# Kernel tuning notes

Hardware: AMD Instinct MI355X
Metric: run time of the kernel (lower is better)

The kernel has to match this reference:

```python
import jax, jax.numpy as jnp
import numpy as np

H = 4       # num_heads
K = 16      # neighbors
EPS = 1e-5  # BatchNorm eps (eval mode with running stats)


def _bn1d(y, g, b, m, v):
    # y: [B, C, N]; per-channel affine batchnorm (eval mode)
    return (y - m[:, None]) * (g[:, None] / jnp.sqrt(v[:, None] + EPS)) + b[:, None]


def setup_inputs() -> dict:
    key = jax.random.key(0)
    ks = jax.random.split(key, 10)
    B, C, N = 2, 256, 4096
    s = 0.02
    inp = {
        'x': jax.random.normal(ks[0], (B, C, N), jnp.float32),
        'xyz': jax.random.normal(ks[1], (B, 3, N), jnp.float32),
        'Wq': jax.random.normal(ks[2], (C, C), jnp.float32) * s,
        'Wkv': jax.random.normal(ks[3], (2 * C, C), jnp.float32) * s,
        'Wproj': jax.random.normal(ks[4], (C, C), jnp.float32) * s,
        'rp_w1': jax.random.normal(ks[5], (C, 3), jnp.float32) * s,
        'rp_g': jnp.ones((C,), jnp.float32),
        'rp_b': jnp.zeros((C,), jnp.float32),
        'rp_m': jnp.zeros((C,), jnp.float32),
        'rp_v': jnp.ones((C,), jnp.float32),
        'rp_w2': jax.random.normal(ks[6], (C, C), jnp.float32) * s,
        'bn1_g': jnp.ones((C,), jnp.float32), 'bn1_b': jnp.zeros((C,), jnp.float32),
        'bn1_m': jnp.zeros((C,), jnp.float32), 'bn1_v': jnp.ones((C,), jnp.float32),
        'bn2_g': jnp.ones((C,), jnp.float32), 'bn2_b': jnp.zeros((C,), jnp.float32),
        'bn2_m': jnp.zeros((C,), jnp.float32), 'bn2_v': jnp.ones((C,), jnp.float32),
        'ffn_w1': jax.random.normal(ks[7], (4 * C, C), jnp.float32) * s,
        'ffn_b1': jnp.zeros((4 * C,), jnp.float32),
        'ffn_w2': jax.random.normal(ks[8], (C, 4 * C), jnp.float32) * s,
        'ffn_b2': jnp.zeros((C,), jnp.float32),
    }
    return inp


def reference(x, xyz, Wq, Wkv, Wproj, rp_w1, rp_g, rp_b, rp_m, rp_v, rp_w2,
              bn1_g, bn1_b, bn1_m, bn1_v, bn2_g, bn2_b, bn2_m, bn2_v,
              ffn_w1, ffn_b1, ffn_w2, ffn_b2):
    B, C, N = x.shape
    d = C // H
    scale = d ** -0.5

    # --- KNN indices ---
    pts = xyz.transpose(0, 2, 1)                       # [B,N,3]
    sq = jnp.sum(pts * pts, -1)                        # [B,N]
    dists = sq[:, :, None] + sq[:, None, :] - 2.0 * jnp.einsum('bnc,bmc->bnm', pts, pts)
    idx = jax.lax.top_k(-dists, K)[1]                  # [B,N,K]

    # --- q, k, v (1x1 conv == matmul over channels) ---
    q = jnp.einsum('oc,bcn->bon', Wq, x).reshape(B, H, d, N)
    kv = jnp.einsum('oc,bcn->bon', Wkv, x)
    kf = kv[:, :C].transpose(0, 2, 1)                  # [B,N,C]
    vf = kv[:, C:].transpose(0, 2, 1)                  # [B,N,C]

    gather = jax.vmap(lambda f, i: f[i])               # per-batch KNN gather
    kg = gather(kf, idx).reshape(B, N, K, H, d)
    vg = gather(vf, idx).reshape(B, N, K, H, d)

    # --- attention logits: per-neighbor dot ---
    logits = jnp.einsum('bhdn,bnkhd->bhnk', q, kg) * scale

    # --- relative-position bias (1x1 conv MLP over rel coords) ---
    nbr = gather(pts, idx)                             # [B,N,K,3]
    rel = nbr - pts[:, :, None, :]                     # [B,N,K,3]
    h1 = jnp.einsum('oc,bnkc->bnko', rp_w1, rel)
    h1 = (h1 - rp_m) * (rp_g / jnp.sqrt(rp_v + EPS)) + rp_b
    h1 = jax.nn.relu(h1)
    h2 = jnp.einsum('oc,bnkc->bnko', rp_w2, h1).reshape(B, N, K, H, d)
    logits = logits + jnp.einsum('bnkhd->bhnk', h2)    # sum over d

    attn = jax.nn.softmax(logits, axis=-1)             # [B,H,N,K]
    out = jnp.einsum('bhnk,bnkhd->bhdn', attn, vg).reshape(B, C, N)
    out = jnp.einsum('oc,bcn->bon', Wproj, out)

    x1 = _bn1d(x + out, bn1_g, bn1_b, bn1_m, bn1_v)
    h = jax.nn.relu(jnp.einsum('oc,bcn->bon', ffn_w1, x1) + ffn_b1[:, None])
    f = jnp.einsum('oc,bcn->bon', ffn_w2, h) + ffn_b2[:, None]
    return _bn1d(x1 + f, bn2_g, bn2_b, bn2_m, bn2_v)
```

## Files before the change

### kernel.cpp

```cpp
#include <hip/hip_runtime.h>
#include <math.h>

#define BB   2
#define CC   256
#define NPT  4096
#define HH   4
#define DD   64
#define KNN  16
#define EPSBN 1e-5f

typedef __attribute__((ext_vector_type(8))) short short8;
typedef __attribute__((ext_vector_type(4))) float f32x4;

typedef __attribute__((address_space(3))) unsigned int lds_u32;
typedef const __attribute__((address_space(1))) unsigned int glb_u32;
__device__ __forceinline__ void gl_lds16(const void* g, void* l) {
  __builtin_amdgcn_global_load_lds((glb_u32*)g, (lds_u32*)l, 16, 0, 0);
}

__device__ __forceinline__ unsigned short f2b(float f) {
  union { float f; unsigned int u; } v; v.f = f;
  unsigned int r = (v.u + 0x7FFFu + ((v.u >> 16) & 1u)) >> 16;
  return (unsigned short)r;
}
__device__ __forceinline__ void up2(unsigned int u, float& a, float& b) {
  union { unsigned int x; float f; } lo, hi;
  lo.x = u << 16; hi.x = u & 0xffff0000u;
  a = lo.f; b = hi.f;
}
__device__ __forceinline__ void up16(uint4 u0, uint4 u1, float* f) {
  up2(u0.x, f[0], f[1]);  up2(u0.y, f[2], f[3]);
  up2(u0.z, f[4], f[5]);  up2(u0.w, f[6], f[7]);
  up2(u1.x, f[8], f[9]);  up2(u1.y, f[10], f[11]);
  up2(u1.z, f[12], f[13]); up2(u1.w, f[14], f[15]);
}

__device__ __forceinline__ unsigned int med3u(unsigned int a, unsigned int b, unsigned int c) {
  unsigned int d;
  asm("v_med3_u32 %0, %1, %2, %3" : "=v"(d) : "v"(a), "v"(b), "v"(c));
  return d;
}

__device__ __forceinline__
void wcast_body(const float* Wq, const float* Wkv, const float* Wp,
                const float* W1, const float* W2,
                unsigned short* oQKV, unsigned short* oP,
                unsigned short* o1, unsigned short* o2,
                const float* rp_w1, const float* rp_g, const float* rp_b,
                const float* rp_m, const float* rp_v, const float* rp_w2,
                float4* w1f, float4* W2t, int blk) {
  if (blk == 3072) {
    int c = threadIdx.x;
    float s  = rp_g[c] / sqrtf(rp_v[c] + EPSBN);
    float b0 = rp_b[c] - rp_m[c] * s;
    w1f[c] = make_float4(rp_w1[c*3+0]*s, rp_w1[c*3+1]*s, rp_w1[c*3+2]*s, b0);
    float a0=0.f,a1=0.f,a2=0.f,a3=0.f;
    for (int o = 0; o < 64; o++) {
      a0 += rp_w2[(      o)*CC + c];
      a1 += rp_w2[( 64 + o)*CC + c];
      a2 += rp_w2[(128 + o)*CC + c];
      a3 += rp_w2[(192 + o)*CC + c];
    }
    W2t[c] = make_float4(a0,a1,a2,a3);
    return;
  }
  int i = blk * 256 + threadIdx.x;
  if (i < 65536)        oQKV[i] = f2b(Wq[i]);
  else if (i < 196608)  oQKV[i] = f2b(Wkv[i - 65536]);
  else if (i < 262144)  oP[i - 196608] = f2b(Wp[i - 196608]);
  else if (i < 524288)  o1[i - 262144] = f2b(W1[i - 262144]);
  else                  o2[i - 524288] = f2b(W2[i - 524288]);
}

__device__ __forceinline__
void xcast_body(const float* x, unsigned short* xb, float* xf,
                float (*T)[65], int bx, int by, int bz) {
  int n0 = bx * 64, c0 = by * 64, bb = bz;
  int tid = threadIdx.x;
  {
    int crow = tid >> 2, ns = (tid & 3) * 16;
    const float* xp = x + ((size_t)(bb*CC + c0 + crow))*NPT + n0 + ns;
#pragma unroll
    for (int i = 0; i < 4; i++) {
      float4 v = ((const float4*)xp)[i];
      T[crow][ns + i*4 + 0] = v.x; T[crow][ns + i*4 + 1] = v.y;
      T[crow][ns + i*4 + 2] = v.z; T[crow][ns + i*4 + 3] = v.w;
    }
  }
  __syncthreads();
  {
    int nrow = tid >> 2, cs = (tid & 3) * 16;
    float vals[16];
#pragma unroll
    for (int i = 0; i < 16; i++) vals[i] = T[cs + i][nrow];
    size_t orow = ((size_t)(bb*NPT + n0 + nrow))*CC + c0 + cs;
#pragma unroll
    for (int i = 0; i < 4; i++)
      *(float4*)&xf[orow + i*4] = make_float4(vals[i*4], vals[i*4+1], vals[i*4+2], vals[i*4+3]);
    unsigned short us[16];
#pragma unroll
    for (int i = 0; i < 16; i++) us[i] = f2b(vals[i]);
    *(uint4*)&xb[orow]     = *(const uint4*)&us[0];
    *(uint4*)&xb[orow + 8] = *(const uint4*)&us[8];
  }
}

#define MPROC(M4, MI) { \
    float nd = fmaf(qx2, (M4).x, fmaf(qy2, (M4).y, fmaf(qz2, (M4).z, (M4).w + qsq))); \
    nd = fmaxf(nd, 0.f); \
    unsigned int key = (__float_as_uint(nd) & 0xFFFFFE00u) | (unsigned int)(MI); \
    k15 = med3u(key, k14, k15); k14 = med3u(key, k13, k14); \
    k13 = med3u(key, k12, k13); k12 = med3u(key, k11, k12); \
    k11 = med3u(key, k10, k11); k10 = med3u(key, k9,  k10); \
    k9  = med3u(key, k8,  k9 ); k8  = med3u(key, k7,  k8 ); \
    k7  = med3u(key, k6,  k7 ); k6  = med3u(key, k5,  k6 ); \
    k5  = med3u(key, k4,  k5 ); k4  = med3u(key, k3,  k4 ); \
    k3  = med3u(key, k2,  k3 ); k2  = med3u(key, k1,  k2 ); \
    k1  = med3u(key, k0,  k1 ); k0  = min(key, k0); }

__device__ __forceinline__
void knn_partial_body(const float* xyz, unsigned int* Pp, float4* sp,
                      int s, int qg, int b) {
  const float* base = xyz + (size_t)b * 3 * NPT;
  int c0 = s * 512;
  for (int i = threadIdx.x; i < 512; i += 256) {
    float mx = base[c0 + i], my = base[NPT + c0 + i], mz = base[2*NPT + c0 + i];
    sp[i] = make_float4(mx, my, mz, mx*mx + my*my + mz*mz);
  }
  int lane = threadIdx.x & 63;
  int wv   = threadIdx.x >> 6;
  int qn   = qg * 64 + lane;
  float qx = base[qn], qy = base[NPT + qn], qz = base[2*NPT + qn];
  float qsq = qx*qx + qy*qy + qz*qz;
  float qx2 = -2.f*qx, qy2 = -2.f*qy, qz2 = -2.f*qz;
  __syncthreads();

  unsigned int k0=0xFFFFFFFFu,k1=0xFFFFFFFFu,k2=0xFFFFFFFFu,k3=0xFFFFFFFFu,
               k4=0xFFFFFFFFu,k5=0xFFFFFFFFu,k6=0xFFFFFFFFu,k7=0xFFFFFFFFu,
               k8=0xFFFFFFFFu,k9=0xFFFFFFFFu,k10=0xFFFFFFFFu,k11=0xFFFFFFFFu,
               k12=0xFFFFFFFFu,k13=0xFFFFFFFFu,k14=0xFFFFFFFFu,k15=0xFFFFFFFFu;

  int sb = wv * 128;
  for (int mm = 0; mm < 128; mm += 4) {
    float4 a = sp[sb+mm], bq = sp[sb+mm+1], cq = sp[sb+mm+2], dq = sp[sb+mm+3];
    MPROC(a,  sb+mm)
    MPROC(bq, sb+mm+1)
    MPROC(cq, sb+mm+2)
    MPROC(dq, sb+mm+3)
  }

  int gq = b * NPT + qn;
  uint4* out = (uint4*)(Pp + (size_t)gq * 512 + (size_t)(s*4 + wv) * 16);
  out[0] = make_uint4(k0,  k1,  k2,  k3);
  out[1] = make_uint4(k4,  k5,  k6,  k7);
  out[2] = make_uint4(k8,  k9,  k10, k11);
  out[3] = make_uint4(k12, k13, k14, k15);
}

__global__ __launch_bounds__(256) __attribute__((amdgpu_waves_per_eu(1, 4)))
void stage1_kernel(const float* x, unsigned short* xb, float* xf,
                   const float* xyz, unsigned int* Pp,
                   const float* Wq, const float* Wkv, const float* Wp,
                   const float* W1, const float* W2,
                   unsigned short* oQKV, unsigned short* oP,
                   unsigned short* o1, unsigned short* o2,
                   const float* rp_w1, const float* rp_g, const float* rp_b,
                   const float* rp_m, const float* rp_v, const float* rp_w2,
                   float4* w1f, float4* W2t) {
  __shared__ __align__(16) char smem[64*65*4];
  int bi = blockIdx.x;
  if (bi < 1024) {
    knn_partial_body(xyz, Pp, (float4*)smem, bi & 7, (bi >> 3) & 63, bi >> 9);
  } else if (bi < 1536) {
    int i = bi - 1024;
    xcast_body(x, xb, xf, (float(*)[65])smem, i & 63, (i >> 6) & 3, i >> 8);
  } else {
    wcast_body(Wq, Wkv, Wp, W1, W2, oQKV, oP, o1, o2,
               rp_w1, rp_g, rp_b, rp_m, rp_v, rp_w2, w1f, W2t, bi - 1536);
  }
}

__device__ __forceinline__
void knn_merge_body(const unsigned int* Pp, int* idx_out, int blk) {
  int wv   = threadIdx.x >> 6;
  int lane = threadIdx.x & 63;
  int gq   = blk * 4 + wv;
  float d[8]; int ii[8];
  const uint4* base = (const uint4*)(Pp + (size_t)gq * 512);
  int gbase = (lane >> 3) * 512;
  {
    uint4 v0 = base[lane*2], v1 = base[lane*2 + 1];
    unsigned int ks[8] = {v0.x, v0.y, v0.z, v0.w, v1.x, v1.y, v1.z, v1.w};
#pragma unroll
    for (int t = 0; t < 8; t++) {
      d[t]  = __uint_as_float(ks[t] & 0xFFFFFE00u);
      ii[t] = gbase + (int)(ks[t] & 0x1FFu);
    }
  }
  for (int sel = 0; sel < 16; sel++) {
    float bd = 3.5e38f; int bi = 0x7fffffff;
#pragma unroll
    for (int t = 0; t < 8; t++) {
      bool better = (d[t] < bd) || (d[t] == bd && ii[t] < bi);
      if (better) { bd = d[t]; bi = ii[t]; }
    }
#pragma unroll
    for (int off = 1; off < 64; off <<= 1) {
      float od = __shfl_xor(bd, off, 64);
      int   oi = __shfl_xor(bi, off, 64);
      if (od < bd || (od == bd && oi < bi)) { bd = od; bi = oi; }
    }
#pragma unroll
    for (int t = 0; t < 8; t++)
      if (ii[t] == bi) d[t] = 3.5e38f;
    if (lane == 0) idx_out[gq*16 + sel] = bi;
  }
}

struct MG {
  const unsigned short* A; const unsigned short* Wt; int K; int M;
  unsigned short* OutB; float* OutF;
  const float* bias; const float* resid;
  const float* bng; const float* bnb; const float* bnm; const float* bnv;
};

template<int EPI, int NT>
__device__ __forceinline__ void mgemm_body(const MG& p, int bx, int by, int bz) {
  __shared__ unsigned short As[NT*64*64];
  __shared__ unsigned short Bs[64*64];
  const int tid  = threadIdx.x;
  const int bb   = bz;
  const int n0   = bx * (NT*64);
  const int m0   = by * 64;
  const int lane = tid & 63;
  const int wv   = tid >> 6;
  const int l15  = lane & 15;
  const int quad = lane >> 4;
  const int K    = p.K;
  const int WR   = NT*16;

  f32x4 acc[NT][4];
#pragma unroll
  for (int i = 0; i < NT; i++)
#pragma unroll
    for (int j = 0; j < 4; j++) acc[i][j] = (f32x4){0.f, 0.f, 0.f, 0.f};

  const int srow = wv*8 + (lane >> 3);
  const int pseg = lane & 7;
  const unsigned short* Abase = p.A  + (size_t)bb*NPT*K;

  for (int c0 = 0; c0 < K; c0 += 64) {
#pragma unroll
    for (int t = 0; t < NT*2; t++) {
      int row = t*32 + srow;
      int ls  = pseg ^ (row & 7);
      gl_lds16(Abase + (size_t)(n0 + row)*K + c0 + ls*8,
               &As[wv*512 + t*2048 + lane*8]);
    }
#pragma unroll
    for (int t = 0; t < 2; t++) {
      int row = t*32 + srow;
      int ls  = pseg ^ (row & 7);
      gl_lds16(p.Wt + (size_t)(m0 + row)*K + c0 + ls*8,
               &Bs[wv*512 + t*2048 + lane*8]);
    }
    __syncthreads();
    short8 bf[4][2];
#pragma unroll
    for (int mt = 0; mt < 4; mt++)
#pragma unroll
      for (int kk = 0; kk < 2; kk++) {
        int row = mt*16 + l15;
        int ps  = (kk*4 + quad) ^ (row & 7);
        bf[mt][kk] = *(const short8*)&Bs[row*64 + ps*8];
      }
#pragma unroll
    for (int nt = 0; nt < NT; nt++)
#pragma unroll
      for (int kk = 0; kk < 2; kk++) {
        int row = wv*WR + nt*16 + l15;
        int ps  = (kk*4 + quad) ^ (row & 7);
        short8 af = *(const short8*)&As[row*64 + ps*8];
#pragma unroll
        for (int mt = 0; mt < 4; mt++)
          acc[nt][mt] = __builtin_amdgcn_mfma_f32_16x16x32_bf16(af, bf[mt][kk], acc[nt][mt], 0, 0, 0);
      }
    __syncthreads();
  }

  if (EPI == 0 || EPI == 1) {
    float bs[4];
#pragma unroll
    for (int mt = 0; mt < 4; mt++)
      bs[mt] = (EPI == 1) ? p.bias[m0 + mt*16 + l15] : 0.f;
#pragma unroll
    for (int nt = 0; nt < NT; nt++)
#pragma unroll
      for (int reg = 0; reg < 4; reg++) {
        size_t row = ((size_t)(bb*NPT + n0 + wv*WR + nt*16 + quad*4 + reg))*p.M + m0;
#pragma unroll
        for (int mt = 0; mt < 4; mt++) {
          float v = acc[nt][mt][reg] + bs[mt];
          if (EPI == 1) v = fmaxf(v, 0.f);
          p.OutB[row + mt*16 + l15] = f2b(v);
        }
      }
  } else if (EPI == 2) {
    float sc[4], sh[4];
#pragma unroll
    for (int mt = 0; mt < 4; mt++) {
      int m = m0 + mt*16 + l15;
      float s = p.bng[m] / sqrtf(p.bnv[m] + EPSBN);
      sc[mt] = s; sh[mt] = p.bnb[m] - p.bnm[m]*s;
    }
#pragma unroll
    for (int nt = 0; nt < NT; nt++)
#pragma unroll
      for (int reg = 0; reg < 4; reg++) {
        size_t row = ((size_t)(bb*NPT + n0 + wv*WR + nt*16 + quad*4 + reg))*p.M + m0;
#pragma unroll
        for (int mt = 0; mt < 4; mt++) {
          float r = p.resid[row + mt*16 + l15];
          float v = (acc[nt][mt][reg] + r)*sc[mt] + sh[mt];
          p.OutF[row + mt*16 + l15] = v;
          p.OutB[row + mt*16 + l15] = f2b(v);
        }
      }
  } else {
    __shared__ float Tb[4][4][16*17];
    float sc[4], sh[4], bs[4];
#pragma unroll
    for (int mt = 0; mt < 4; mt++) {
      int m = m0 + mt*16 + l15;
      float s = p.bng[m] / sqrtf(p.bnv[m] + EPSBN);
      sc[mt] = s; sh[mt] = p.bnb[m] - p.bnm[m]*s;
      bs[mt] = p.bias[m];
    }
#pragma unroll
    for (int nt = 0; nt < NT; nt++) {
#pragma unroll
      for (int reg = 0; reg < 4; reg++) {
        size_t row = ((size_t)(bb*NPT + n0 + wv*WR + nt*16 + quad*4 + reg))*p.M + m0;
#pragma unroll
        for (int mt = 0; mt < 4; mt++) {
          float r = p.resid[row + mt*16 + l15];
          float v = (acc[nt][mt][reg] + bs[mt] + r)*sc[mt] + sh[mt];
          Tb[wv][mt][(quad*4 + reg)*17 + l15] = v;
        }
      }
      __syncthreads();
#pragma unroll
      for (int mt = 0; mt < 4; mt++)
#pragma unroll
        for (int reg = 0; reg < 4; reg++) {
          float v = Tb[wv][mt][l15*17 + quad*4 + reg];
          p.OutF[((size_t)(bb*p.M + m0 + mt*16 + quad*4 + reg))*NPT
                 + n0 + wv*WR + nt*16 + l15] = v;
        }
      __syncthreads();
    }
  }
}

template<int EPI, int NT>
__global__ __launch_bounds__(256)
void mgemm_kernel(MG p) { mgemm_body<EPI, NT>(p, blockIdx.x, blockIdx.y, blockIdx.z); }

__global__ __launch_bounds__(256)
void stage2_kernel(const unsigned int* Pp, int* idx, MG pqkv) {
  int bi = blockIdx.x;
  if (bi < 2048) {
    knn_merge_body(Pp, idx, bi);
  } else {
    int i = bi - 2048;
    mgemm_body<0, 2>(pqkv, i & 31, (i >> 5) % 12, i / 384);
  }
}

__global__ __launch_bounds__(256, 4)
void attn_kernel(const unsigned short* __restrict__ qkv, const float4* __restrict__ w1f,
                 const float4* __restrict__ W2t, const float* __restrict__ xyz,
                 const int* __restrict__ idx, unsigned short* __restrict__ attn_b) {
  __shared__ float4 sw1[256];
  __shared__ float4 sw2[256];
  __shared__ int   sidx[4][16];
  __shared__ float srel[4][16][4];
  __shared__ float sbias[4][16][4];
  __shared__ float red[4][16*68];
  int tid = threadIdx.x;
  int bn0 = blockIdx.x * 4;
  int b   = bn0 >> 12;
  sw1[tid] = w1f[tid];
  sw2[tid] = W2t[tid];
  if (tid < 64) {
    int p = tid >> 4, kk = tid & 15;
    int bn = bn0 + p, n = bn & 4095;
    int j = idx[bn*16 + kk];
    sidx[p][kk] = j;
    const float* pb = xyz + (size_t)b * 3 * NPT;
    srel[p][kk][0] = pb[j]         - pb[n];
    srel[p][kk][1] = pb[NPT + j]   - pb[NPT + n];
    srel[p][kk][2] = pb[2*NPT + j] - pb[2*NPT + n];
  }
  __syncthreads();
  {
    int kk = tid >> 4, cs = tid & 15;
    float rx[4], ry[4], rz[4], h[4][4];
#pragma unroll
    for (int p = 0; p < 4; p++) {
      rx[p] = srel[p][kk][0]; ry[p] = srel[p][kk][1]; rz[p] = srel[p][kk][2];
#pragma unroll
      for (int q = 0; q < 4; q++) h[p][q] = 0.f;
    }
#pragma unroll
    for (int i = 0; i < 16; i++) {
      int c = cs*16 + ((i + cs) & 15);
      float4 w  = sw1[c];
      float4 w2 = sw2[c];
#pragma unroll
      for (int p = 0; p < 4; p++) {
        float t0 = fmaxf(fmaf(rx[p], w.x, fmaf(ry[p], w.y, fmaf(rz[p], w.z, w.w))), 0.f);
        h[p][0] = fmaf(t0, w2.x, h[p][0]); h[p][1] = fmaf(t0, w2.y, h[p][1]);
        h[p][2] = fmaf(t0, w2.z, h[p][2]); h[p][3] = fmaf(t0, w2.w, h[p][3]);
      }
    }
#pragma unroll
    for (int off = 1; off < 16; off <<= 1)
#pragma unroll
      for (int p = 0; p < 4; p++)
#pragma unroll
        for (int q = 0; q < 4; q++)
          h[p][q] += __shfl_xor(h[p][q], off, 64);
    if (cs == 0)
#pragma unroll
      for (int p = 0; p < 4; p++)
#pragma unroll
        for (int q = 0; q < 4; q++) sbias[p][kk][q] = h[p][q];
  }
  __syncthreads();
  int wv   = tid >> 6;
  int lane = tid & 63;
  int k    = lane >> 2;
  int c4   = lane & 3;
  int ch0  = wv*64 + c4*16;
  size_t base = (size_t)(b*NPT) * 768;
#pragma unroll 1
  for (int p = 0; p < 4; p++) {
    int bn = bn0 + p;
    size_t rowq = (size_t)bn * 768;
    float qf[16];
    {
      uint4 q0 = *(const uint4*)(qkv + rowq + ch0);
      uint4 q1 = *(const uint4*)(qkv + rowq + ch0 + 8);
      up16(q0, q1, qf);
    }
    int j = sidx[p][k];
    float dot = 0.f;
    {
      const unsigned short* krow = qkv + base + (size_t)j*768 + 256 + ch0;
      uint4 k0 = *(const uint4*)(krow);
      uint4 k1 = *(const uint4*)(krow + 8);
      float kf[16];
      up16(k0, k1, kf);
#pragma unroll
      for (int i = 0; i < 16; i++) dot = fmaf(qf[i], kf[i], dot);
    }
    dot += __shfl_xor(dot, 1, 64);
    dot += __shfl_xor(dot, 2, 64);
    float logit = dot * 0.125f + sbias[p][k][wv];
    float mx = logit;
#pragma unroll
    for (int off = 4; off < 64; off <<= 1) mx = fmaxf(mx, __shfl_xor(mx, off, 64));
    float e = __expf(logit - mx);
    float ssum = e;
#pragma unroll
    for (int off = 4; off < 64; off <<= 1) ssum += __shfl_xor(ssum, off, 64);
    float w = e / ssum;
    {
      const unsigned short* vrow = qkv + base + (size_t)j*768 + 512 + ch0;
      uint4 v0 = *(const uint4*)(vrow);
      uint4 v1 = *(const uint4*)(vrow + 8);
      float vf[16];
      up16(v0, v1, vf);
      float* dst = &red[wv][k*68 + c4*16];
#pragma unroll
      for (int g = 0; g < 4; g++)
        ((float4*)dst)[g] = make_float4(w*vf[g*4], w*vf[g*4+1], w*vf[g*4+2], w*vf[g*4+3]);
    }
    __syncthreads();
    float o = 0.f;
#pragma unroll
    for (int kk2 = 0; kk2 < 16; kk2++) o += red[wv][kk2*68 + lane];
    attn_b[(size_t)bn*256 + wv*64 + lane] = f2b(o);
    __syncthreads();
  }
}

extern "C" void kernel_launch(void* const* d_in, const int* in_sizes, int n_in,
                              void* d_out, int out_size, void* d_ws, size_t ws_size,
                              hipStream_t stream) {
  const float* x     = (const float*)d_in[0];
  const float* xyz   = (const float*)d_in[1];
  const float* Wq    = (const float*)d_in[2];
  const float* Wkv   = (const float*)d_in[3];
  const float* Wproj = (const float*)d_in[4];
  const float* rp_w1 = (const float*)d_in[5];
  const float* rp_g  = (const float*)d_in[6];
  const float* rp_b  = (const float*)d_in[7];
  const float* rp_m  = (const float*)d_in[8];
  const float* rp_v  = (const float*)d_in[9];
  const float* rp_w2 = (const float*)d_in[10];
  const float* bn1_g = (const float*)d_in[11];
  const float* bn1_b = (const float*)d_in[12];
  const float* bn1_m = (const float*)d_in[13];
  const float* bn1_v = (const float*)d_in[14];
  const float* bn2_g = (const float*)d_in[15];
  const float* bn2_b = (const float*)d_in[16];
  const float* bn2_m = (const float*)d_in[17];
  const float* bn2_v = (const float*)d_in[18];
  const float* ffn_w1 = (const float*)d_in[19];
  const float* ffn_b1 = (const float*)d_in[20];
  const float* ffn_w2 = (const float*)d_in[21];
  const float* ffn_b2 = (const float*)d_in[22];

  char* ws = (char*)d_ws;
  float4* w1f = (float4*)(ws + 0);
  float4* W2t = (float4*)(ws + 4096);
  int*    idx = (int*)  (ws + 8192);
  const size_t oA = 532480;
  unsigned int*   Pp     = (unsigned int*)(ws + oA);
  unsigned short* attn_b = (unsigned short*)(ws + oA);
  float*          x1f    = (float*)(ws + oA + (4u<<20));
  unsigned short* x1b    = (unsigned short*)(ws + oA + (12u<<20));
  unsigned short* h_b    = (unsigned short*)(ws + oA + (16u<<20));
  const size_t oB = oA + (32u<<20);
  unsigned short* Wqkv_b  = (unsigned short*)(ws + oB);
  unsigned short* Wproj_b = (unsigned short*)(ws + oB + 393216);
  unsigned short* W1_b    = (unsigned short*)(ws + oB + 524288);
  unsigned short* W2_b    = (unsigned short*)(ws + oB + 1048576);
  unsigned short* xb      = (unsigned short*)(ws + oB + 1572864);
  float*          xf      = (float*)(ws + oB + 1572864 + (4u<<20));
  unsigned short* qkv     = (unsigned short*)(ws + oB + 1572864 + (12u<<20));

  stage1_kernel<<<4609, 256, 0, stream>>>(x, xb, xf, xyz, Pp,
                                          Wq, Wkv, Wproj, ffn_w1, ffn_w2,
                                          Wqkv_b, Wproj_b, W1_b, W2_b,
                                          rp_w1, rp_g, rp_b, rp_m, rp_v, rp_w2,
                                          w1f, W2t);

  MG pqkv = {xb, Wqkv_b, 256, 768, qkv, nullptr,
             nullptr, nullptr, nullptr, nullptr, nullptr, nullptr};
  stage2_kernel<<<2816, 256, 0, stream>>>(Pp, idx, pqkv);

  attn_kernel<<<(BB*NPT)/4, 256, 0, stream>>>(qkv, w1f, W2t, xyz, idx, attn_b);

  MG pproj = {attn_b, Wproj_b, 256, 256, x1b, x1f,
              nullptr, xf, bn1_g, bn1_b, bn1_m, bn1_v};
  mgemm_kernel<2, 1><<<dim3(64, 4, BB), 256, 0, stream>>>(pproj);

  MG pf1 = {x1b, W1_b, 256, 1024, h_b, nullptr,
            ffn_b1, nullptr, nullptr, nullptr, nullptr, nullptr};
  mgemm_kernel<1, 2><<<dim3(32, 16, BB), 256, 0, stream>>>(pf1);

  MG pf2 = {h_b, W2_b, 1024, 256, nullptr, (float*)d_out,
            ffn_b2, x1f, bn2_g, bn2_b, bn2_m, bn2_v};
  mgemm_kernel<3, 1><<<dim3(64, 4, BB), 256, 0, stream>>>(pf2);
}
```

Measured before the change: 230.1 us.

## Replace iterative argmin KNN merge with bitonic merge of packed 64-bit keys

The KNN merge stage used to pick the 16 nearest neighbours with 16 sequential rounds of per-lane argmin followed by a wave-wide shuffle reduction. It now packs distance and index into one 64-bit key and keeps a sorted list of 16 keys per lane. Lists are merged across lanes with six butterfly rounds, each a min-merge plus a bitonic clean-up. This removes the serial select loop and writes the indices with vector stores, at the cost of more registers and 64-bit shuffles. Correctness depends on each lane's partial candidates already being sorted ascending.

```diff
diff --git a/kernel.cpp b/kernel.cpp
--- a/kernel.cpp
+++ b/kernel.cpp
@@ -180,40 +180,61 @@
   }
 }
 
+__device__ __forceinline__ unsigned long long min64(unsigned long long a, unsigned long long b) {
+  return a < b ? a : b;
+}
+__device__ __forceinline__ void ce64(unsigned long long& x, unsigned long long& y) {
+  unsigned long long a = x, b = y;
+  bool lt = a < b;
+  x = lt ? a : b;
+  y = lt ? b : a;
+}
 __device__ __forceinline__
 void knn_merge_body(const unsigned int* Pp, int* idx_out, int blk) {
   int wv   = threadIdx.x >> 6;
   int lane = threadIdx.x & 63;
   int gq   = blk * 4 + wv;
-  float d[8]; int ii[8];
   const uint4* base = (const uint4*)(Pp + (size_t)gq * 512);
-  int gbase = (lane >> 3) * 512;
+  uint4 v0 = base[lane*2], v1 = base[lane*2 + 1];
+  unsigned int gb = (unsigned int)(lane >> 3) * 512u;
+  unsigned long long a[16];
   {
-    uint4 v0 = base[lane*2], v1 = base[lane*2 + 1];
     unsigned int ks[8] = {v0.x, v0.y, v0.z, v0.w, v1.x, v1.y, v1.z, v1.w};
 #pragma unroll
-    for (int t = 0; t < 8; t++) {
-      d[t]  = __uint_as_float(ks[t] & 0xFFFFFE00u);
-      ii[t] = gbase + (int)(ks[t] & 0x1FFu);
-    }
-  }
-  for (int sel = 0; sel < 16; sel++) {
-    float bd = 3.5e38f; int bi = 0x7fffffff;
-#pragma unroll
-    for (int t = 0; t < 8; t++) {
-      bool better = (d[t] < bd) || (d[t] == bd && ii[t] < bi);
-      if (better) { bd = d[t]; bi = ii[t]; }
-    }
-#pragma unroll
-    for (int off = 1; off < 64; off <<= 1) {
-      float od = __shfl_xor(bd, off, 64);
-      int   oi = __shfl_xor(bi, off, 64);
-      if (od < bd || (od == bd && oi < bi)) { bd = od; bi = oi; }
-    }
-#pragma unroll
     for (int t = 0; t < 8; t++)
-      if (ii[t] == bi) d[t] = 3.5e38f;
-    if (lane == 0) idx_out[gq*16 + sel] = bi;
+      a[t] = ((unsigned long long)(ks[t] & 0xFFFFFE00u) << 32) | (gb + (ks[t] & 0x1FFu));
+#pragma unroll
+    for (int t = 8; t < 16; t++) a[t] = ~0ull;
+  }
+#pragma unroll
+  for (int r = 0; r < 6; r++) {
+    const int m = 1 << r;
+    unsigned long long t[16];
+#pragma unroll
+    for (int i = 0; i < 16; i++) {
+      unsigned long long pb = __shfl_xor(a[15 - i], m, 64);
+      t[i] = min64(a[i], pb);
+    }
+    if (r < 5) {
+#pragma unroll
+      for (int d = 8; d >= 1; d >>= 1)
+#pragma unroll
+        for (int i = 0; i < 16; i++)
+          if ((i & d) == 0) ce64(t[i], t[i + d]);
+    }
+#pragma unroll
+    for (int i = 0; i < 16; i++) a[i] = t[i];
+  }
+  if (lane == 0) {
+    int4* o = (int4*)(idx_out + gq*16);
+    o[0] = make_int4((int)(unsigned)a[0],  (int)(unsigned)a[1],
+                     (int)(unsigned)a[2],  (int)(unsigned)a[3]);
+    o[1] = make_int4((int)(unsigned)a[4],  (int)(unsigned)a[5],
+                     (int)(unsigned)a[6],  (int)(unsigned)a[7]);
+    o[2] = make_int4((int)(unsigned)a[8],  (int)(unsigned)a[9],
+                     (int)(unsigned)a[10], (int)(unsigned)a[11]);
+    o[3] = make_int4((int)(unsigned)a[12], (int)(unsigned)a[13],
+                     (int)(unsigned)a[14], (int)(unsigned)a[15]);
   }
 }
 
```

Result: faster. 222.1 us (-3.5%).
